# Performance work log

Hardware: AMD Instinct MI355X
Metric: run time of the kernel (lower is better)

Reference implementation:

```python
import jax, jax.numpy as jnp
import numpy as np
import math

IMG_H = 360; IMG_W = 640; S = 72; STRIDE = 8
FH = IMG_H // STRIDE  # 45
FW = IMG_W // STRIDE  # 80
C_IN = 64; C_FEAT = 64
B = 16


def _make_anchors():
    # Replicates LaneATTHead._generate_anchors with lateral_n=72, bottom_n=128.
    anchor_ys = np.linspace(1.0, 0.0, S)
    cut_ys = np.linspace(1.0, 0.0, FH)
    left = [72., 60., 49., 39., 30., 22.]
    right = [108., 120., 131., 141., 150., 158.]
    bottom = [165., 150., 141., 131., 120., 108., 100., 90., 80., 72., 60., 49., 39., 30., 15.]

    def side(angles, nb, x=None, y=None):
        if y is not None:
            sx0 = np.linspace(1.0, 0.0, nb); sy0 = np.full(nb, y)
        else:
            sx0 = np.full(nb, x); sy0 = np.linspace(1.0, 0.0, nb)
        na = len(angles)
        sx = np.repeat(sx0, na); sy = np.repeat(sy0, na)  # start index outer, angle inner
        t = np.tile(np.tan(np.array(angles) * math.pi / 180.0), nb)
        def build(ys):
            a = np.zeros((nb * na, 5 + len(ys)), dtype=np.float32)
            a[:, 2] = 1.0 - sy
            a[:, 3] = sx
            a[:, 5:] = (sx[:, None] + (sy[:, None] - ys[None, :]) / t[:, None]) * IMG_W
            return a
        return build(anchor_ys), build(cut_ys)

    la, lc = side(left, 72, x=0.0)
    ra, rc = side(right, 72, x=1.0)
    ba, bc = side(bottom, 128, y=1.0)
    anchors = np.concatenate([la, ba, ra], axis=0)       # (2784, 77)
    anchors_cut = np.concatenate([lc, bc, rc], axis=0)   # (2784, 50)
    return anchors, anchors_cut


def setup_inputs() -> dict:
    key = jax.random.key(0)
    ks = jax.random.split(key, 4)
    anchors, cuts = _make_anchors()
    scale = IMG_W / FW
    xs = np.round(cuts[:, 5:] / scale).astype(np.int64)
    xs = np.ascontiguousarray(xs[:, ::-1])               # flip along fmap-y
    invalid = (xs < 0) | (xs >= FW)
    xs = np.clip(xs, 0, FW - 1)
    feat_dim = C_FEAT * FH  # 2880
    return {
        "x": jax.random.normal(ks[0], (B, C_IN, FH, FW), jnp.float32),
        "conv_w": jax.random.normal(ks[1], (C_FEAT, C_IN), jnp.float32) * math.sqrt(2.0 / C_FEAT),
        "conv_b": jnp.zeros((C_FEAT,), jnp.float32),
        "cls_w": jax.random.normal(ks[2], (feat_dim, 2), jnp.float32) * 0.01,
        "cls_b": jnp.zeros((2,), jnp.float32),
        "reg_w": jax.random.normal(ks[3], (feat_dim, S + 1), jnp.float32) * 0.01,
        "reg_b": jnp.zeros((S + 1,), jnp.float32),
        "anchors": jnp.asarray(anchors),
        "cut_xs": jnp.asarray(xs, jnp.int32),            # (N, FH)
        "invalid_mask": jnp.asarray(invalid),            # (N, FH) bool
    }


def reference(x, conv_w, conv_b, cls_w, cls_b, reg_w, reg_b, anchors, cut_xs, invalid_mask):
    Bn = x.shape[0]
    N = anchors.shape[0]
    # 1x1 conv
    feat = jnp.einsum('bchw,oc->bohw', x, conv_w) + conv_b[None, :, None, None]
    # anchor feature cutting: out[b,c,n,y] = feat[b,c,y,cut_xs[n,y]]
    ys = jnp.arange(FH)
    g = feat[:, :, ys[None, :], cut_xs]                  # (B, C, N, FH)
    g = jnp.where(invalid_mask[None, None], 0.0, g)
    f = g.transpose(0, 2, 1, 3).reshape(Bn, N, C_FEAT * FH)  # (B, N, 2880), C outer then fh
    cls_logits = f @ cls_w + cls_b                       # (B, N, 2)
    reg = f @ reg_w + reg_b                              # (B, N, 73)
    p24 = jnp.broadcast_to(anchors[None, :, 2:4], (Bn, N, 2))
    out = jnp.concatenate([cls_logits, p24, anchors[None, :, 4:] + reg], axis=-1)  # (B, N, 77)
    return out
```

## Files before the change

kernel.cpp:

```cpp
#include <hip/hip_runtime.h>
#include <hip/hip_bf16.h>
#include <stdint.h>

#define FH 45
#define FW 80
#define CIN 64
#define CF 64
#define NANCH 2784
#define BB 16
#define JP 80
#define JN 75
#define MROW (FH * FW)
#define SB ((MROW + 1) * JP)
#define ZOFF (MROW * JP)
#define TOTBN (BB * NANCH)
#define ANB 25
#define CPB ((NANCH + ANB - 1) / ANB)

static __device__ __forceinline__ uint32_t pkbf(float a, float b) {
    uint32_t lo = (uint32_t)__bfloat16_as_ushort(__float2bfloat16(a));
    uint32_t hi = (uint32_t)__bfloat16_as_ushort(__float2bfloat16(b));
    return lo | (hi << 16);
}

__global__ __launch_bounds__(256) void k1_weights(
    const float* __restrict__ conv_w, const float* __restrict__ conv_b,
    const float* __restrict__ cls_w, const float* __restrict__ reg_w,
    const int* __restrict__ cut_xs, const uint8_t* __restrict__ invalid,
    float* __restrict__ V, float* __restrict__ biasM, int* __restrict__ off) {
    int blk = blockIdx.x;
    int tid = threadIdx.x;
    if (blk >= 90) {
        int idx = (blk - 90) * 256 + tid;
        if (idx < NANCH * FH) {
            int y = idx % FH;
            off[idx] = invalid[idx] ? ZOFF : (y * FW + cut_xs[idx]) * JP;
        }
        return;
    }
    int y = blk >> 1;
    int j0 = (blk & 1) * 40;
    __shared__ float cw[CF * CIN];
    __shared__ float wl[CF * 40];
    __shared__ float cb[CF];
    for (int i = tid; i < CF * CIN; i += 256) cw[i] = conv_w[i];
    if (tid < CF) cb[tid] = conv_b[tid];
    for (int i = tid; i < CF * 40; i += 256) {
        int c = i / 40, jl = i % 40, j = j0 + jl;
        float v = 0.f;
        if (j < 2) v = cls_w[(c * FH + y) * 2 + j];
        else if (j < JN) v = reg_w[(c * FH + y) * 73 + (j - 2)];
        wl[i] = v;
    }
    __syncthreads();
    int ci = tid & 63;
    int jb = tid >> 6;
    float acc[10];
    #pragma unroll
    for (int k = 0; k < 10; ++k) acc[k] = 0.f;
    for (int c = 0; c < CF; ++c) {
        float a = cw[c * CIN + ci];
        #pragma unroll
        for (int k = 0; k < 10; ++k)
            acc[k] = fmaf(a, wl[c * 40 + jb + 4 * k], acc[k]);
    }
    #pragma unroll
    for (int k = 0; k < 10; ++k)
        V[y * (CIN * JP) + ci * JP + j0 + jb + 4 * k] = acc[k];
    if (tid < 40) {
        float s = 0.f;
        for (int c = 0; c < CF; ++c) s += cb[c] * wl[c * 40 + tid];
        biasM[y * JP + j0 + tid] = s;
    }
}

__global__ __launch_bounds__(256) void k2_feat(
    const float* __restrict__ x, const float* __restrict__ V,
    const float* __restrict__ biasM, __hip_bfloat16* __restrict__ M) {
    int b = blockIdx.x / FH;
    int y = blockIdx.x % FH;
    __shared__ float xl[CIN * FW];
    __shared__ float vl[CIN * JP];
    __shared__ float bl[JP];
    int tid = threadIdx.x;
    for (int t = tid; t < CIN * FW; t += 256) {
        int ci = t / FW, xc = t % FW;
        xl[t] = x[((b * CIN + ci) * FH + y) * FW + xc];
    }
    const float* vsrc = V + y * (CIN * JP);
    for (int t = tid; t < CIN * JP; t += 256) vl[t] = vsrc[t];
    if (tid < JP) bl[tid] = biasM[y * JP + tid];
    __hip_bfloat16* Mb = M + (size_t)b * SB;
    if (y == 0 && tid < JP) Mb[ZOFF + tid] = __float2bfloat16(0.f);
    __syncthreads();
    if (tid < 200) {
        int tx = tid % 20;
        int tj = tid / 20;
        int x0 = tx * 4, jg0 = tj * 8;
        float acc[4][8];
        for (int xx = 0; xx < 4; ++xx)
            for (int jj = 0; jj < 8; ++jj)
                acc[xx][jj] = bl[jg0 + jj];
        for (int ci = 0; ci < CIN; ++ci) {
            float4 xv = *reinterpret_cast<const float4*>(&xl[ci * FW + x0]);
            float4 v0 = *reinterpret_cast<const float4*>(&vl[ci * JP + jg0]);
            float4 v1 = *reinterpret_cast<const float4*>(&vl[ci * JP + jg0 + 4]);
            float xa[4] = {xv.x, xv.y, xv.z, xv.w};
            float va[8] = {v0.x, v0.y, v0.z, v0.w, v1.x, v1.y, v1.z, v1.w};
            for (int xx = 0; xx < 4; ++xx)
                for (int jj = 0; jj < 8; ++jj)
                    acc[xx][jj] = fmaf(xa[xx], va[jj], acc[xx][jj]);
        }
        __hip_bfloat16* mbase = Mb + ((size_t)y * FW) * JP;
        for (int xx = 0; xx < 4; ++xx) {
            uint32_t* row = (uint32_t*)(mbase + (size_t)(x0 + xx) * JP + jg0);
            uint4 pk;
            pk.x = pkbf(acc[xx][0], acc[xx][1]);
            pk.y = pkbf(acc[xx][2], acc[xx][3]);
            pk.z = pkbf(acc[xx][4], acc[xx][5]);
            pk.w = pkbf(acc[xx][6], acc[xx][7]);
            *reinterpret_cast<uint4*>(row) = pk;
        }
    }
}

__global__ __launch_bounds__(256) void k3_gather(
    const __hip_bfloat16* __restrict__ M, const float* __restrict__ anchors,
    const float* __restrict__ cls_b, const float* __restrict__ reg_b,
    const int* __restrict__ off, float* __restrict__ out) {
    __shared__ int sidx[ANB * FH];
    int tid = threadIdx.x;
    int wg = blockIdx.x;
    int b = (wg % 8) * 2 + ((wg >> 3) & 1);
    int chunk = wg >> 4;
    int n0 = chunk * ANB;
    int nvalid = NANCH - n0; if (nvalid > ANB) nvalid = ANB;
    for (int i = tid; i < ANB * FH; i += 256) {
        int nl = i / FH;
        sidx[i] = (nl < nvalid) ? off[n0 * FH + i] : ZOFF;
    }
    __syncthreads();
    if (tid >= ANB * 10) return;
    int lb = tid / 10;
    int jg = tid % 10;
    if (lb >= nvalid) return;
    int n = n0 + lb;
    const __hip_bfloat16* mb = M + (size_t)b * SB + jg * 8;
    const int* si = sidx + lb * FH;
    float s[8];
    #pragma unroll
    for (int e = 0; e < 8; ++e) s[e] = 0.f;
    #pragma unroll
    for (int y = 0; y < FH; ++y) {
        int o = si[y];
        uint4 v = *reinterpret_cast<const uint4*>(mb + o);
        uint32_t u[4] = {v.x, v.y, v.z, v.w};
        #pragma unroll
        for (int p = 0; p < 4; ++p) {
            s[2 * p]     += __uint_as_float(u[p] << 16);
            s[2 * p + 1] += __uint_as_float(u[p] & 0xFFFF0000u);
        }
    }
    float* dst = out + ((size_t)b * NANCH + n) * 77;
    const float* arow = anchors + (size_t)n * 77;
    int j0 = jg * 8;
    #pragma unroll
    for (int e = 0; e < 8; ++e) {
        int j = j0 + e;
        if (j < 2)       dst[j]     = s[e] + cls_b[j];
        else if (j < JN) dst[j + 2] = s[e] + reg_b[j - 2] + arow[j + 2];
    }
    if (jg == 0) { dst[2] = arow[2]; dst[3] = arow[3]; }
}

extern "C" void kernel_launch(void* const* d_in, const int* in_sizes, int n_in,
                              void* d_out, int out_size, void* d_ws, size_t ws_size,
                              hipStream_t stream) {
    const float* x       = (const float*)d_in[0];
    const float* conv_w  = (const float*)d_in[1];
    const float* conv_b  = (const float*)d_in[2];
    const float* cls_w   = (const float*)d_in[3];
    const float* cls_b   = (const float*)d_in[4];
    const float* reg_w   = (const float*)d_in[5];
    const float* reg_b   = (const float*)d_in[6];
    const float* anchors = (const float*)d_in[7];
    const int* cut_xs    = (const int*)d_in[8];
    const uint8_t* invalid = (const uint8_t*)d_in[9];
    float* out = (float*)d_out;

    float* V     = (float*)d_ws;
    float* biasM = V + FH * CIN * JP;
    __hip_bfloat16* M = (__hip_bfloat16*)(biasM + FH * JP);
    int*   off   = (int*)((char*)M + (size_t)BB * SB * sizeof(__hip_bfloat16));

    int n_off_blocks = (NANCH * FH + 255) / 256;
    k1_weights<<<90 + n_off_blocks, 256, 0, stream>>>(conv_w, conv_b, cls_w, reg_w,
                                                      cut_xs, invalid, V, biasM, off);
    k2_feat<<<BB * FH, 256, 0, stream>>>(x, V, biasM, M);
    k3_gather<<<16 * CPB, 256, 0, stream>>>(M, anchors, cls_b, reg_b, off, out);
}
```

Baseline: 141.9 us.

## Stage gather outputs in LDS, prefetch feature slab, remap batch-to-block order

The gather kernel now stages the anchor rows and biases in shared memory, builds each 25-anchor output tile in LDS, and writes it back with contiguous coalesced stores instead of scattered per-thread stores. Each block also prefetches a slice of its batch's bf16 feature slab into cache before the gather, with a dummy accumulation to keep the loads alive. The feature kernel's block-to-batch mapping is changed to match the gather's interleaved order so that producer and consumer blocks touch the same batches, which may improve L2 or MALL locality. The cost is extra LDS use, an extra barrier, and prefetch traffic that may be wasted.

Result: no change. 143.8 us (+1.3%).

```diff
diff --git a/kernel.cpp b/kernel.cpp
--- a/kernel.cpp
+++ b/kernel.cpp
@@ -13,9 +13,10 @@
 #define MROW (FH * FW)
 #define SB ((MROW + 1) * JP)
 #define ZOFF (MROW * JP)
-#define TOTBN (BB * NANCH)
 #define ANB 25
 #define CPB ((NANCH + ANB - 1) / ANB)
+#define SLAB_BYTES (SB * 2)
+#define PFQ 5376
 
 static __device__ __forceinline__ uint32_t pkbf(float a, float b) {
     uint32_t lo = (uint32_t)__bfloat16_as_ushort(__float2bfloat16(a));
@@ -77,8 +78,9 @@
 __global__ __launch_bounds__(256) void k2_feat(
     const float* __restrict__ x, const float* __restrict__ V,
     const float* __restrict__ biasM, __hip_bfloat16* __restrict__ M) {
-    int b = blockIdx.x / FH;
-    int y = blockIdx.x % FH;
+    int wg = blockIdx.x;
+    int b = (wg % 8) * 2 + ((wg >> 3) & 1);
+    int y = wg >> 4;
     __shared__ float xl[CIN * FW];
     __shared__ float vl[CIN * JP];
     __shared__ float bl[JP];
@@ -129,48 +131,75 @@
     const float* __restrict__ cls_b, const float* __restrict__ reg_b,
     const int* __restrict__ off, float* __restrict__ out) {
     __shared__ int sidx[ANB * FH];
+    __shared__ float sanch[ANB * 77];
+    __shared__ float sout[ANB * 77];
+    __shared__ float sbias[JN];
     int tid = threadIdx.x;
     int wg = blockIdx.x;
     int b = (wg % 8) * 2 + ((wg >> 3) & 1);
     int chunk = wg >> 4;
     int n0 = chunk * ANB;
     int nvalid = NANCH - n0; if (nvalid > ANB) nvalid = ANB;
+
+    const char* slab = (const char*)(M + (size_t)b * SB);
+    int pbase = chunk * PFQ;
+    float keep = 0.f;
+    {
+        int p0 = pbase + tid * 16;
+        if (p0 + 16 <= SLAB_BYTES) {
+            float4 v = *reinterpret_cast<const float4*>(slab + p0);
+            keep += v.x + v.y + v.z + v.w;
+        }
+        int p1 = pbase + 4096 + tid * 16;
+        if (tid < 80 && p1 + 16 <= SLAB_BYTES) {
+            float4 v = *reinterpret_cast<const float4*>(slab + p1);
+            keep += v.x + v.y + v.z + v.w;
+        }
+    }
     for (int i = tid; i < ANB * FH; i += 256) {
         int nl = i / FH;
         sidx[i] = (nl < nvalid) ? off[n0 * FH + i] : ZOFF;
     }
-    __syncthreads();
-    if (tid >= ANB * 10) return;
+    for (int i = tid; i < nvalid * 77; i += 256)
+        sanch[i] = anchors[(size_t)n0 * 77 + i];
+    if (tid < JN) sbias[tid] = (tid < 2) ? cls_b[tid] : reg_b[tid - 2];
+    __syncthreads();
+    asm volatile("" :: "v"(keep));
+
     int lb = tid / 10;
     int jg = tid % 10;
-    if (lb >= nvalid) return;
-    int n = n0 + lb;
-    const __hip_bfloat16* mb = M + (size_t)b * SB + jg * 8;
-    const int* si = sidx + lb * FH;
-    float s[8];
-    #pragma unroll
-    for (int e = 0; e < 8; ++e) s[e] = 0.f;
-    #pragma unroll
-    for (int y = 0; y < FH; ++y) {
-        int o = si[y];
-        uint4 v = *reinterpret_cast<const uint4*>(mb + o);
-        uint32_t u[4] = {v.x, v.y, v.z, v.w};
-        #pragma unroll
-        for (int p = 0; p < 4; ++p) {
-            s[2 * p]     += __uint_as_float(u[p] << 16);
-            s[2 * p + 1] += __uint_as_float(u[p] & 0xFFFF0000u);
-        }
-    }
-    float* dst = out + ((size_t)b * NANCH + n) * 77;
-    const float* arow = anchors + (size_t)n * 77;
-    int j0 = jg * 8;
-    #pragma unroll
-    for (int e = 0; e < 8; ++e) {
-        int j = j0 + e;
-        if (j < 2)       dst[j]     = s[e] + cls_b[j];
-        else if (j < JN) dst[j + 2] = s[e] + reg_b[j - 2] + arow[j + 2];
-    }
-    if (jg == 0) { dst[2] = arow[2]; dst[3] = arow[3]; }
+    if (lb < nvalid && tid < ANB * 10) {
+        const __hip_bfloat16* mb = M + (size_t)b * SB + jg * 8;
+        const int* si = sidx + lb * FH;
+        float s[8];
+        #pragma unroll
+        for (int e = 0; e < 8; ++e) s[e] = 0.f;
+        #pragma unroll
+        for (int y = 0; y < FH; ++y) {
+            int o = si[y];
+            uint4 v = *reinterpret_cast<const uint4*>(mb + o);
+            uint32_t u[4] = {v.x, v.y, v.z, v.w};
+            #pragma unroll
+            for (int p = 0; p < 4; ++p) {
+                s[2 * p]     += __uint_as_float(u[p] << 16);
+                s[2 * p + 1] += __uint_as_float(u[p] & 0xFFFF0000u);
+            }
+        }
+        float* so = sout + lb * 77;
+        const float* sa = sanch + lb * 77;
+        int j0 = jg * 8;
+        #pragma unroll
+        for (int e = 0; e < 8; ++e) {
+            int j = j0 + e;
+            if (j < 2)       so[j]     = s[e] + sbias[j];
+            else if (j < JN) so[j + 2] = s[e] + sbias[j] + sa[j + 2];
+        }
+        if (jg == 0) { so[2] = sa[2]; so[3] = sa[3]; }
+    }
+    __syncthreads();
+    float* dsl = out + ((size_t)b * NANCH + n0) * 77;
+    int tot = nvalid * 77;
+    for (int i = tid; i < tot; i += 256) dsl[i] = sout[i];
 }
 
 extern "C" void kernel_launch(void* const* d_in, const int* in_sizes, int n_in,
```

## Stage per-row feature planes in shared memory with double buffering for anchor gather

Applied to the files above, without the earlier changes.

The gather kernel now walks the 45 feature-map rows one at a time. For each row it loads that row's 80x80 bf16 plane of projected features into shared memory, double-buffered with prefetch of the next row, and 87 anchors per block read their cell from LDS instead of scattered global loads. Offsets are compressed to uint8 column indices, with index 80 pointing at a zeroed padding row, and k2 block ordering is interleaved across batches. This is meant to cut the random global/L2 traffic of the gather. In exchange it adds 45 block-wide barriers per block, uses large 896-thread blocks and about 29KB of LDS, and launches only 512 blocks.

After: 154.4 us. 8.8% more time.

```diff
diff --git a/kernel.cpp b/kernel.cpp
--- a/kernel.cpp
+++ b/kernel.cpp
@@ -12,10 +12,10 @@
 #define JN 75
 #define MROW (FH * FW)
 #define SB ((MROW + 1) * JP)
-#define ZOFF (MROW * JP)
-#define TOTBN (BB * NANCH)
-#define ANB 25
-#define CPB ((NANCH + ANB - 1) / ANB)
+#define ANB3 87
+#define PLROW 44
+#define PLSZ (81 * PLROW)
+#define PLBYTES 12800
 
 static __device__ __forceinline__ uint32_t pkbf(float a, float b) {
     uint32_t lo = (uint32_t)__bfloat16_as_ushort(__float2bfloat16(a));
@@ -27,15 +27,13 @@
     const float* __restrict__ conv_w, const float* __restrict__ conv_b,
     const float* __restrict__ cls_w, const float* __restrict__ reg_w,
     const int* __restrict__ cut_xs, const uint8_t* __restrict__ invalid,
-    float* __restrict__ V, float* __restrict__ biasM, int* __restrict__ off) {
+    float* __restrict__ V, float* __restrict__ biasM, uint8_t* __restrict__ xv) {
     int blk = blockIdx.x;
     int tid = threadIdx.x;
     if (blk >= 90) {
         int idx = (blk - 90) * 256 + tid;
-        if (idx < NANCH * FH) {
-            int y = idx % FH;
-            off[idx] = invalid[idx] ? ZOFF : (y * FW + cut_xs[idx]) * JP;
-        }
+        if (idx < NANCH * FH)
+            xv[idx] = invalid[idx] ? (uint8_t)80 : (uint8_t)cut_xs[idx];
         return;
     }
     int y = blk >> 1;
@@ -77,8 +75,9 @@
 __global__ __launch_bounds__(256) void k2_feat(
     const float* __restrict__ x, const float* __restrict__ V,
     const float* __restrict__ biasM, __hip_bfloat16* __restrict__ M) {
-    int b = blockIdx.x / FH;
-    int y = blockIdx.x % FH;
+    int wg = blockIdx.x;
+    int b = (wg % 8) * 2 + ((wg >> 3) & 1);
+    int y = wg >> 4;
     __shared__ float xl[CIN * FW];
     __shared__ float vl[CIN * JP];
     __shared__ float bl[JP];
@@ -90,8 +89,6 @@
     const float* vsrc = V + y * (CIN * JP);
     for (int t = tid; t < CIN * JP; t += 256) vl[t] = vsrc[t];
     if (tid < JP) bl[tid] = biasM[y * JP + tid];
-    __hip_bfloat16* Mb = M + (size_t)b * SB;
-    if (y == 0 && tid < JP) Mb[ZOFF + tid] = __float2bfloat16(0.f);
     __syncthreads();
     if (tid < 200) {
         int tx = tid % 20;
@@ -102,16 +99,16 @@
             for (int jj = 0; jj < 8; ++jj)
                 acc[xx][jj] = bl[jg0 + jj];
         for (int ci = 0; ci < CIN; ++ci) {
-            float4 xv = *reinterpret_cast<const float4*>(&xl[ci * FW + x0]);
+            float4 xvv = *reinterpret_cast<const float4*>(&xl[ci * FW + x0]);
             float4 v0 = *reinterpret_cast<const float4*>(&vl[ci * JP + jg0]);
             float4 v1 = *reinterpret_cast<const float4*>(&vl[ci * JP + jg0 + 4]);
-            float xa[4] = {xv.x, xv.y, xv.z, xv.w};
+            float xa[4] = {xvv.x, xvv.y, xvv.z, xvv.w};
             float va[8] = {v0.x, v0.y, v0.z, v0.w, v1.x, v1.y, v1.z, v1.w};
             for (int xx = 0; xx < 4; ++xx)
                 for (int jj = 0; jj < 8; ++jj)
                     acc[xx][jj] = fmaf(xa[xx], va[jj], acc[xx][jj]);
         }
-        __hip_bfloat16* mbase = Mb + ((size_t)y * FW) * JP;
+        __hip_bfloat16* mbase = M + (size_t)b * SB + ((size_t)y * FW) * JP;
         for (int xx = 0; xx < 4; ++xx) {
             uint32_t* row = (uint32_t*)(mbase + (size_t)(x0 + xx) * JP + jg0);
             uint4 pk;
@@ -124,53 +121,72 @@
     }
 }
 
-__global__ __launch_bounds__(256) void k3_gather(
+__global__ __launch_bounds__(896) void k3_gather(
     const __hip_bfloat16* __restrict__ M, const float* __restrict__ anchors,
     const float* __restrict__ cls_b, const float* __restrict__ reg_b,
-    const int* __restrict__ off, float* __restrict__ out) {
-    __shared__ int sidx[ANB * FH];
+    const uint8_t* __restrict__ xv, float* __restrict__ out) {
+    __shared__ uint32_t pl[2 * PLSZ];
+    __shared__ uint8_t sx[ANB3 * FH];
+    __shared__ float sbias[JN + 1];
     int tid = threadIdx.x;
     int wg = blockIdx.x;
     int b = (wg % 8) * 2 + ((wg >> 3) & 1);
     int chunk = wg >> 4;
-    int n0 = chunk * ANB;
-    int nvalid = NANCH - n0; if (nvalid > ANB) nvalid = ANB;
-    for (int i = tid; i < ANB * FH; i += 256) {
-        int nl = i / FH;
-        sidx[i] = (nl < nvalid) ? off[n0 * FH + i] : ZOFF;
-    }
+    int n0 = chunk * ANB3;
+    const char* slab = (const char*)(M + (size_t)b * SB);
+
+    for (int i = tid; i < ANB3 * FH; i += 896) sx[i] = xv[n0 * FH + i];
+    if (tid < JN) sbias[tid] = (tid < 2) ? cls_b[tid] : reg_b[tid - 2];
+    if (tid < 2 * PLROW)
+        pl[(tid < PLROW ? 0 : PLSZ) + 80 * PLROW + (tid % PLROW)] = 0u;
+    int xr = tid / 10, w4 = tid % 10;
+    if (tid < 800)
+        *reinterpret_cast<uint4*>(&pl[xr * PLROW + w4 * 4]) =
+            *reinterpret_cast<const uint4*>(slab + tid * 16);
     __syncthreads();
-    if (tid >= ANB * 10) return;
-    int lb = tid / 10;
-    int jg = tid % 10;
-    if (lb >= nvalid) return;
-    int n = n0 + lb;
-    const __hip_bfloat16* mb = M + (size_t)b * SB + jg * 8;
-    const int* si = sidx + lb * FH;
+
+    int anc = tid / 10, jg = tid % 10;
+    bool task = (tid < ANB3 * 10);
+    const uint8_t* sxa = sx + anc * FH;
     float s[8];
     #pragma unroll
     for (int e = 0; e < 8; ++e) s[e] = 0.f;
-    #pragma unroll
+
     for (int y = 0; y < FH; ++y) {
-        int o = si[y];
-        uint4 v = *reinterpret_cast<const uint4*>(mb + o);
-        uint32_t u[4] = {v.x, v.y, v.z, v.w};
+        uint32_t cur = (uint32_t)(y & 1) * PLSZ;
+        uint32_t nxt = PLSZ - cur;
+        uint4 g;
+        bool stg = (y + 1 < FH) && (tid < 800);
+        if (stg)
+            g = *reinterpret_cast<const uint4*>(slab + (size_t)(y + 1) * PLBYTES + tid * 16);
+        if (task) {
+            int xcell = sxa[y];
+            uint4 v = *reinterpret_cast<const uint4*>(&pl[cur + xcell * PLROW + jg * 4]);
+            uint32_t u[4] = {v.x, v.y, v.z, v.w};
+            #pragma unroll
+            for (int p = 0; p < 4; ++p) {
+                s[2 * p]     += __uint_as_float(u[p] << 16);
+                s[2 * p + 1] += __uint_as_float(u[p] & 0xFFFF0000u);
+            }
+        }
+        if (stg)
+            *reinterpret_cast<uint4*>(&pl[nxt + xr * PLROW + w4 * 4]) = g;
+        __syncthreads();
+    }
+
+    if (task) {
+        int n = n0 + anc;
+        float* dst = out + ((size_t)b * NANCH + n) * 77;
+        const float* arow = anchors + (size_t)n * 77;
+        int j0 = jg * 8;
         #pragma unroll
-        for (int p = 0; p < 4; ++p) {
-            s[2 * p]     += __uint_as_float(u[p] << 16);
-            s[2 * p + 1] += __uint_as_float(u[p] & 0xFFFF0000u);
-        }
-    }
-    float* dst = out + ((size_t)b * NANCH + n) * 77;
-    const float* arow = anchors + (size_t)n * 77;
-    int j0 = jg * 8;
-    #pragma unroll
-    for (int e = 0; e < 8; ++e) {
-        int j = j0 + e;
-        if (j < 2)       dst[j]     = s[e] + cls_b[j];
-        else if (j < JN) dst[j + 2] = s[e] + reg_b[j - 2] + arow[j + 2];
-    }
-    if (jg == 0) { dst[2] = arow[2]; dst[3] = arow[3]; }
+        for (int e = 0; e < 8; ++e) {
+            int j = j0 + e;
+            if (j < 2)       dst[j]     = s[e] + sbias[j];
+            else if (j < JN) dst[j + 2] = s[e] + sbias[j] + arow[j + 2];
+        }
+        if (jg == 0) { dst[2] = arow[2]; dst[3] = arow[3]; }
+    }
 }
 
 extern "C" void kernel_launch(void* const* d_in, const int* in_sizes, int n_in,
@@ -191,11 +207,11 @@
     float* V     = (float*)d_ws;
     float* biasM = V + FH * CIN * JP;
     __hip_bfloat16* M = (__hip_bfloat16*)(biasM + FH * JP);
-    int*   off   = (int*)((char*)M + (size_t)BB * SB * sizeof(__hip_bfloat16));
-
-    int n_off_blocks = (NANCH * FH + 255) / 256;
-    k1_weights<<<90 + n_off_blocks, 256, 0, stream>>>(conv_w, conv_b, cls_w, reg_w,
-                                                      cut_xs, invalid, V, biasM, off);
+    uint8_t* xv  = (uint8_t*)((char*)M + (size_t)BB * SB * sizeof(__hip_bfloat16));
+
+    int n_xv_blocks = (NANCH * FH + 255) / 256;
+    k1_weights<<<90 + n_xv_blocks, 256, 0, stream>>>(conv_w, conv_b, cls_w, reg_w,
+                                                     cut_xs, invalid, V, biasM, xv);
     k2_feat<<<BB * FH, 256, 0, stream>>>(x, V, biasM, M);
-    k3_gather<<<16 * CPB, 256, 0, stream>>>(M, anchors, cls_b, reg_b, off, out);
-}
+    k3_gather<<<512, 896, 0, stream>>>(M, anchors, cls_b, reg_b, xv, out);
+}
```
